# Optimization experiments

Measured on AMD Instinct MI355X. Metric: run time of the kernel, lower is better.

The kernel has to match this reference:

```python
import jax, jax.numpy as jnp
import numpy as np

B, S, D, H = 1, 2048, 1024, 16
HD = D // H
S_SLOPE = 10.0      # soft_thres_layer s
C_MASK = -10000.0   # soft_thres_layer c == masked_bias
ALPHA = 0.0         # config.threshold
W_STD = 0.02        # GPT2 init std for weights


def setup_inputs() -> dict:
    key = jax.random.key(0)
    k1, k2, k3 = jax.random.split(key, 3)
    return {
        "hidden_states": jax.random.normal(k1, (B, S, D), dtype=jnp.float32),
        "c_attn_w": jax.random.normal(k2, (D, 3 * D), dtype=jnp.float32) * W_STD,
        "c_attn_b": jnp.zeros((3 * D,), dtype=jnp.float32),
        "c_proj_w": jax.random.normal(k3, (D, D), dtype=jnp.float32) * W_STD,
        "c_proj_b": jnp.zeros((D,), dtype=jnp.float32),
    }


def reference(hidden_states, c_attn_w, c_attn_b, c_proj_w, c_proj_b):
    # Conv1D: x @ w + b (GPT2 convention: weight is [in, out])
    qkv = hidden_states @ c_attn_w + c_attn_b            # [B,S,3D]
    q, k, v = jnp.split(qkv, 3, axis=-1)

    def split_heads(x):
        return x.reshape(B, S, H, HD).transpose(0, 2, 1, 3)  # [B,H,S,hd]

    q, k, v = split_heads(q), split_heads(k), split_heads(v)

    # prun path: NO 1/sqrt(d) scaling (skipped when self.prun is True)
    w = jnp.einsum("bhqd,bhkd->bhqk", q, k)              # [B,H,S,S]

    causal = jnp.tril(jnp.ones((S, S), dtype=bool))[None, None]
    w = jnp.where(causal, w, C_MASK)

    # soft-threshold pruning: smoothly pushes scores below alpha toward c=-10000
    w = C_MASK + (w - C_MASK) * jax.nn.sigmoid(S_SLOPE * (w - ALPHA))

    a = jax.nn.softmax(w, axis=-1)                        # attn_dropout = identity (eval)
    out = jnp.einsum("bhqk,bhkd->bhqd", a, v)             # [B,H,S,hd]
    out = out.transpose(0, 2, 1, 3).reshape(B, S, D)      # merge heads
    return out @ c_proj_w + c_proj_b                      # resid_dropout = identity
```

## Files before the change

### kernel.cpp

```cpp
#include <hip/hip_runtime.h>


#define S_LEN 2048
#define DM    1024
#define NH    16
#define HD    64
#define SLOPE 10.0f
#define CMASK -10000.0f
#define SP    2080

typedef short s16x4 __attribute__((ext_vector_type(4)));
typedef short s16x8 __attribute__((ext_vector_type(8)));
typedef float f32x4 __attribute__((ext_vector_type(4)));

#define MFMA16(a,b,c) __builtin_amdgcn_mfma_f32_16x16x32_bf16(a,b,c,0,0,0)
#define GLDS16(g,l) __builtin_amdgcn_global_load_lds( \
    (const __attribute__((address_space(1))) void*)(g), \
    (__attribute__((address_space(3))) void*)(l), 16, 0, 0)

__device__ __forceinline__ short f2bf(float f){
    unsigned u = __float_as_uint(f);
    u += 0x7fffu + ((u >> 16) & 1u);
    return (short)(u >> 16);
}
__device__ __forceinline__ float bf2f(short x){
    return __uint_as_float(((unsigned)(unsigned short)x) << 16);
}
struct bfpair { short hi, lo; };
__device__ __forceinline__ bfpair split_bf(float x){
    bfpair r; r.hi = f2bf(x);
    r.lo = f2bf(x - bf2f(r.hi));
    return r;
}

template<int ROWS, int THREADS>
__device__ __forceinline__ void stage_tile(const short* gbase, int rstride,
                                           short* lds, int tid){
#pragma unroll
    for (int it = 0; it < ROWS*8/THREADS; ++it){
        int s = it*THREADS + tid;
        int row = s >> 3, grp = s & 7;
        const short* src = gbase + (size_t)row*rstride + ((grp ^ (row & 7)) << 3);
        GLDS16(src, lds + (size_t)s*8);
    }
}
__device__ __forceinline__ s16x8 frag(const short* lds, int row, int kg){
    return *(const s16x8*)&lds[row*64 + ((kg ^ (row & 7)) << 3)];
}

__global__ __launch_bounds__(256)
void gemm_qkv(const short* __restrict__ Ahg, const short* __restrict__ Alg,
              const short* __restrict__ Bhg, const short* __restrict__ Blg,
              const float* __restrict__ bias,
              short* __restrict__ QHh, short* __restrict__ QHl,
              short* __restrict__ KH,  short* __restrict__ Vb)
{
    __shared__ __align__(16) short Ah_s[128*64];
    __shared__ __align__(16) short Bh_s[128*64];
    __shared__ __align__(16) short Al_s[128*64];
    __shared__ __align__(16) short Bl_s[128*64];

    const int tid = threadIdx.x, lane = tid & 63, wid = tid >> 6;
    const int lr = lane & 15, lg = lane >> 4;
    const int brow = blockIdx.y*128, bcol = blockIdx.x*128;
    const int sec = bcol >> 10;
    const int wm = (wid >> 1)*64, wn = (wid & 1)*64;

    f32x4 acc[4][4];
#pragma unroll
    for (int m = 0; m < 4; ++m)
#pragma unroll
        for (int n = 0; n < 4; ++n) acc[m][n] = (f32x4){0.f,0.f,0.f,0.f};

    for (int k0 = 0; k0 < DM; k0 += 64){
        stage_tile<128,256>(Ahg + (size_t)brow*DM + k0, DM, Ah_s, tid);
        stage_tile<128,256>(Bhg + (size_t)bcol*DM + k0, DM, Bh_s, tid);
        if (sec == 0){
            stage_tile<128,256>(Alg + (size_t)brow*DM + k0, DM, Al_s, tid);
            stage_tile<128,256>(Blg + (size_t)bcol*DM + k0, DM, Bl_s, tid);
        }
        __syncthreads();
#pragma unroll
        for (int kc = 0; kc < 2; ++kc){
            s16x8 ah[4], al[4], bh[4], bl[4];
#pragma unroll
            for (int m = 0; m < 4; ++m)
                ah[m] = frag(Ah_s, wm + m*16 + lr, kc*4 + lg);
#pragma unroll
            for (int n = 0; n < 4; ++n)
                bh[n] = frag(Bh_s, wn + n*16 + lr, kc*4 + lg);
            if (sec == 0){
#pragma unroll
                for (int m = 0; m < 4; ++m)
                    al[m] = frag(Al_s, wm + m*16 + lr, kc*4 + lg);
#pragma unroll
                for (int n = 0; n < 4; ++n)
                    bl[n] = frag(Bl_s, wn + n*16 + lr, kc*4 + lg);
            }
#pragma unroll
            for (int m = 0; m < 4; ++m)
#pragma unroll
                for (int n = 0; n < 4; ++n){
                    acc[m][n] = MFMA16(ah[m], bh[n], acc[m][n]);
                    if (sec == 0){
                        acc[m][n] = MFMA16(ah[m], bl[n], acc[m][n]);
                        acc[m][n] = MFMA16(al[m], bh[n], acc[m][n]);
                    }
                }
        }
        __syncthreads();
    }

#pragma unroll
    for (int m = 0; m < 4; ++m)
#pragma unroll
        for (int n = 0; n < 4; ++n){
            int row  = brow + wm + m*16 + lg*4;
            int gcol = bcol + wn + n*16 + lr;
            float bv = bias[gcol];
            int h0 = (gcol & 1023) >> 6, d = gcol & 63;
#pragma unroll
            for (int v = 0; v < 4; ++v){
                float val = acc[m][n][v] + bv;
                if (sec == 0){
                    bfpair p = split_bf(val);
                    size_t o = ((size_t)h0*S_LEN + row + v)*HD + d;
                    QHh[o] = p.hi; QHl[o] = p.lo;
                } else if (sec == 1){
                    KH[((size_t)h0*S_LEN + row + v)*HD + d] = f2bf(val);
                } else {
                    Vb[(size_t)(row + v)*DM + (gcol & 1023)] = f2bf(val);
                }
            }
        }
}

__global__ __launch_bounds__(256)
void gemm_proj(const short* __restrict__ Ahg, const short* __restrict__ Bhg,
               const float* __restrict__ bias, float* __restrict__ C)
{
    __shared__ __align__(16) short Ah_s[128*64];
    __shared__ __align__(16) short Bh_s[128*64];

    const int tid = threadIdx.x, lane = tid & 63, wid = tid >> 6;
    const int lr = lane & 15, lg = lane >> 4;
    const int brow = blockIdx.y*128, bcol = blockIdx.x*128;
    const int wm = (wid >> 1)*64, wn = (wid & 1)*64;

    f32x4 acc[4][4];
#pragma unroll
    for (int m = 0; m < 4; ++m)
#pragma unroll
        for (int n = 0; n < 4; ++n) acc[m][n] = (f32x4){0.f,0.f,0.f,0.f};

    for (int k0 = 0; k0 < DM; k0 += 64){
        stage_tile<128,256>(Ahg + (size_t)brow*DM + k0, DM, Ah_s, tid);
        stage_tile<128,256>(Bhg + (size_t)bcol*DM + k0, DM, Bh_s, tid);
        __syncthreads();
#pragma unroll
        for (int kc = 0; kc < 2; ++kc){
            s16x8 ah[4], bh[4];
#pragma unroll
            for (int m = 0; m < 4; ++m)
                ah[m] = frag(Ah_s, wm + m*16 + lr, kc*4 + lg);
#pragma unroll
            for (int n = 0; n < 4; ++n)
                bh[n] = frag(Bh_s, wn + n*16 + lr, kc*4 + lg);
#pragma unroll
            for (int m = 0; m < 4; ++m)
#pragma unroll
                for (int n = 0; n < 4; ++n)
                    acc[m][n] = MFMA16(ah[m], bh[n], acc[m][n]);
        }
        __syncthreads();
    }

#pragma unroll
    for (int m = 0; m < 4; ++m)
#pragma unroll
        for (int n = 0; n < 4; ++n){
            int row  = brow + wm + m*16 + lg*4;
            int gcol = bcol + wn + n*16 + lr;
            float bv = bias[gcol];
#pragma unroll
            for (int v = 0; v < 4; ++v)
                C[(size_t)(row + v)*DM + gcol] = acc[m][n][v] + bv;
        }
}

__global__ __launch_bounds__(256)
void split_f32(const float* __restrict__ x, short* __restrict__ h,
               short* __restrict__ l, int n4)
{
    int i = blockIdx.x*256 + threadIdx.x;
    if (i >= n4) return;
    float4 v = *(const float4*)&x[(size_t)i*4];
    bfpair a = split_bf(v.x), b = split_bf(v.y), c = split_bf(v.z), d = split_bf(v.w);
    s16x4 hv, lv;
    hv.x = a.hi; hv.y = b.hi; hv.z = c.hi; hv.w = d.hi;
    lv.x = a.lo; lv.y = b.lo; lv.z = c.lo; lv.w = d.lo;
    *(s16x4*)&h[(size_t)i*4] = hv;
    *(s16x4*)&l[(size_t)i*4] = lv;
}

template<bool SPL>
__global__ __launch_bounds__(256)
void wtrans(const float* __restrict__ W, int N, short* __restrict__ Th,
            short* __restrict__ Tl)
{
    __shared__ float t[64][65];
    const int tid = threadIdx.x;
    const int tn = blockIdx.x*64, tk = blockIdx.y*64;
#pragma unroll
    for (int it = 0; it < 4; ++it){
        int idx = tid + it*256;
        int r = idx >> 4, c4 = (idx & 15)*4;
        float4 v = *(const float4*)&W[(size_t)(tk + r)*N + tn + c4];
        t[r][c4] = v.x; t[r][c4+1] = v.y; t[r][c4+2] = v.z; t[r][c4+3] = v.w;
    }
    __syncthreads();
#pragma unroll
    for (int it = 0; it < 4; ++it){
        int idx = tid + it*256;
        int n = idx >> 4, c4 = (idx & 15)*4;
        s16x4 hv, lv;
#pragma unroll
        for (int j = 0; j < 4; ++j){
            bfpair p = split_bf(t[c4+j][n]);
            hv[j] = p.hi; lv[j] = p.lo;
        }
        *(s16x4*)&Th[(size_t)(tn + n)*DM + tk + c4] = hv;
        if (SPL && tn < DM)
            *(s16x4*)&Tl[(size_t)(tn + n)*DM + tk + c4] = lv;
    }
}

__global__ __launch_bounds__(256)
void vtrans(const short* __restrict__ Vb, short* __restrict__ Vt)
{
    __shared__ short t[64][66];
    const int tid = threadIdx.x;
    const int td = blockIdx.x*64, ts = blockIdx.y*64;
#pragma unroll
    for (int it = 0; it < 4; ++it){
        int idx = tid + it*256;
        int r = idx >> 4, c4 = (idx & 15)*4;
        s16x4 v = *(const s16x4*)&Vb[(size_t)(ts + r)*DM + td + c4];
        t[r][c4] = v.x; t[r][c4+1] = v.y; t[r][c4+2] = v.z; t[r][c4+3] = v.w;
    }
    __syncthreads();
#pragma unroll
    for (int it = 0; it < 4; ++it){
        int idx = tid + it*256;
        int n = idx >> 4, c4 = (idx & 15)*4;
        s16x4 o;
#pragma unroll
        for (int j = 0; j < 4; ++j) o[j] = t[c4+j][n];
        *(s16x4*)&Vt[(size_t)(td + n)*SP + ts + c4] = o;
    }
}

__global__ __launch_bounds__(64)
void sv_partial(const short* __restrict__ Vb, float* __restrict__ PB)
{
    int b = blockIdx.x, h = blockIdx.y, d = threadIdx.x;
    float s = 0.f;
#pragma unroll 8
    for (int k = 0; k < 64; ++k)
        s += bf2f(Vb[(size_t)(b*64 + k)*DM + h*HD + d]);
    PB[((size_t)h*32 + b)*64 + d] = s;
}
__global__ __launch_bounds__(64)
void sv_suffix(const float* __restrict__ PB, float* __restrict__ SSV)
{
    int h = blockIdx.x, d = threadIdx.x;
    float s = 0.f;
    SSV[((size_t)h*33 + 32)*64 + d] = 0.f;
    for (int b = 31; b >= 0; --b){
        s += PB[((size_t)h*32 + b)*64 + d];
        SSV[((size_t)h*33 + b)*64 + d] = s;
    }
}

__global__ __launch_bounds__(64)
void attn_chunk(const short* __restrict__ QHh, const short* __restrict__ QHl,
                const short* __restrict__ KH, const short* __restrict__ Vt,
                short* __restrict__ acc0, short* __restrict__ acc1,
                short* __restrict__ acc2, float* __restrict__ ML)
{
    __shared__ __align__(16) short Ps[16*72];

    const int j = blockIdx.x;
    const int h = (j & 7) + 8*((j >> 3) & 1);
    const int t = j >> 4;
    const int g = (t < 32) ? 0 : (t < 96) ? 1 : (t < 192) ? 2 : 3;
    const int u = t - 16*g*(g+1);
    const int qd = u / (g+1);
    const int qt = 32*g + qd;
    const int chunk = u - qd*(g+1);
    const int diag = qt >> 2;
    const int kv0 = chunk*8;
    const int kv1 = min(kv0 + 8, diag + 1);

    const int lane = threadIdx.x, lr = lane & 15, lg = lane >> 4;
    const int qrow = qt*16 + lg*4;

    const short* qbh = QHh + ((size_t)h*S_LEN + qt*16)*HD;
    const short* qbl = QHl + ((size_t)h*S_LEN + qt*16)*HD;
    s16x8 aqh[2], aql[2];
#pragma unroll
    for (int kc = 0; kc < 2; ++kc){
        aqh[kc] = *(const s16x8*)&qbh[lr*HD + kc*32 + lg*8];
        aql[kc] = *(const s16x8*)&qbl[lr*HD + kc*32 + lg*8];
    }

    float m_run[4], l_run[4];
    f32x4 acc_o[4];
#pragma unroll
    for (int v = 0; v < 4; ++v){ m_run[v] = -1e30f; l_run[v] = 0.f; }
#pragma unroll
    for (int n = 0; n < 4; ++n) acc_o[n] = (f32x4){0.f,0.f,0.f,0.f};

    const short* kb0 = KH + (size_t)h*S_LEN*HD;
    const short* vb0 = Vt + (size_t)(h*HD)*SP;

    for (int kvb = kv0; kvb < kv1; ++kvb){
        const short* kb = kb0 + (size_t)(kvb*64)*HD;
        s16x8 bk[2][4];
#pragma unroll
        for (int kc = 0; kc < 2; ++kc)
#pragma unroll
            for (int n = 0; n < 4; ++n)
                bk[kc][n] = *(const s16x8*)&kb[(n*16 + lr)*HD + kc*32 + lg*8];

        f32x4 sc[4];
#pragma unroll
        for (int n = 0; n < 4; ++n) sc[n] = (f32x4){0.f,0.f,0.f,0.f};
#pragma unroll
        for (int kc = 0; kc < 2; ++kc)
#pragma unroll
            for (int n = 0; n < 4; ++n){
                sc[n] = MFMA16(aqh[kc], bk[kc][n], sc[n]);
                sc[n] = MFMA16(aql[kc], bk[kc][n], sc[n]);
            }

        const short* vb = vb0 + kvb*64;
        s16x8 bv0[4], bv1[4];
#pragma unroll
        for (int n = 0; n < 4; ++n){
            bv0[n] = *(const s16x8*)&vb[(size_t)(16*n + lr)*SP + lg*8];
            bv1[n] = *(const s16x8*)&vb[(size_t)(16*n + lr)*SP + 32 + lg*8];
        }

        float p[4][4], tmax[4];
#pragma unroll
        for (int v = 0; v < 4; ++v) tmax[v] = -1e30f;
        if (kvb == diag){
#pragma unroll
            for (int n = 0; n < 4; ++n){
                int key = kvb*64 + n*16 + lr;
#pragma unroll
                for (int v = 0; v < 4; ++v){
                    float w;
                    if (key > qrow + v) w = CMASK;
                    else {
                        float sv = sc[n][v];
                        float sig = 1.f / (1.f + __expf(-SLOPE*sv));
                        w = CMASK + (sv - CMASK)*sig;
                    }
                    p[n][v] = w;
                    tmax[v] = fmaxf(tmax[v], w);
                }
            }
        } else {
#pragma unroll
            for (int n = 0; n < 4; ++n)
#pragma unroll
                for (int v = 0; v < 4; ++v){
                    float sv = sc[n][v];
                    float sig = 1.f / (1.f + __expf(-SLOPE*sv));
                    float w = CMASK + (sv - CMASK)*sig;
                    p[n][v] = w;
                    tmax[v] = fmaxf(tmax[v], w);
                }
        }
#pragma unroll
        for (int v = 0; v < 4; ++v)
#pragma unroll
            for (int msk = 1; msk < 16; msk <<= 1)
                tmax[v] = fmaxf(tmax[v], __shfl_xor(tmax[v], msk, 64));

        float scale[4], rsum[4];
#pragma unroll
        for (int v = 0; v < 4; ++v){
            float mn = fmaxf(m_run[v], tmax[v]);
            scale[v] = __expf(m_run[v] - mn);
            m_run[v] = mn;
            rsum[v] = 0.f;
        }
#pragma unroll
        for (int n = 0; n < 4; ++n)
#pragma unroll
            for (int v = 0; v < 4; ++v){
                float e = __expf(p[n][v] - m_run[v]);
                p[n][v] = e;
                rsum[v] += e;
            }
#pragma unroll
        for (int v = 0; v < 4; ++v){
#pragma unroll
            for (int msk = 1; msk < 16; msk <<= 1)
                rsum[v] += __shfl_xor(rsum[v], msk, 64);
            l_run[v] = l_run[v]*scale[v] + rsum[v];
        }
#pragma unroll
        for (int n = 0; n < 4; ++n)
#pragma unroll
            for (int v = 0; v < 4; ++v) acc_o[n][v] *= scale[v];

#pragma unroll
        for (int n = 0; n < 4; ++n)
#pragma unroll
            for (int v = 0; v < 4; ++v)
                Ps[(lg*4 + v)*72 + 16*n + lr] = f2bf(p[n][v]);
        asm volatile("s_waitcnt lgkmcnt(0)" ::: "memory");

        s16x8 pa0 = *(const s16x8*)&Ps[lr*72 + lg*8];
        s16x8 pa1 = *(const s16x8*)&Ps[lr*72 + 32 + lg*8];
#pragma unroll
        for (int n = 0; n < 4; ++n){
            acc_o[n] = MFMA16(pa0, bv0[n], acc_o[n]);
            acc_o[n] = MFMA16(pa1, bv1[n], acc_o[n]);
        }
    }

    short* ab = (j < 2048) ? acc0 + (size_t)j*1024
              : (j < 3072) ? acc1 + (size_t)(j-2048)*1024
                           : acc2 + (size_t)(j-3072)*1024;
#pragma unroll
    for (int n = 0; n < 4; ++n)
#pragma unroll
        for (int v = 0; v < 4; ++v)
            ab[(lg*4 + v)*64 + 16*n + lr] = f2bf(acc_o[n][v]);
    if (lr == 0){
#pragma unroll
        for (int v = 0; v < 4; ++v){
            ML[((size_t)j*16 + lg*4 + v)*2 + 0] = m_run[v];
            ML[((size_t)j*16 + lg*4 + v)*2 + 1] = l_run[v];
        }
    }
}

__global__ __launch_bounds__(64)
void attn_merge(const short* __restrict__ acc0, const short* __restrict__ acc1,
                const short* __restrict__ acc2, const float* __restrict__ ML,
                const float* __restrict__ SSV, short* __restrict__ O)
{
    const int b = blockIdx.x;
    const int h = b & 15, qt = b >> 4;
    const int d = threadIdx.x;
    const int g = qt >> 5, C = g + 1;
    const int tbase = (g + 1)*(qt - 16*g);
    const int diag = qt >> 2;
    const float F = (float)(S_LEN - 64*(diag + 1));
    const float svd = SSV[((size_t)h*33 + (diag + 1))*64 + d];

    for (int r = 0; r < 16; ++r){
        float M = -1e30f;
        for (int c = 0; c < C; ++c){
            int job = (tbase + c)*16 + h;
            M = fmaxf(M, ML[((size_t)job*16 + r)*2]);
        }
        float num = 0.f, den = 0.f;
        for (int c = 0; c < C; ++c){
            int job = (tbase + c)*16 + h;
            float m = ML[((size_t)job*16 + r)*2];
            float l = ML[((size_t)job*16 + r)*2 + 1];
            const short* ab = (job < 2048) ? acc0 + (size_t)job*1024
                            : (job < 3072) ? acc1 + (size_t)(job-2048)*1024
                                           : acc2 + (size_t)(job-3072)*1024;
            float e = __expf(m - M);
            num += e * bf2f(ab[r*64 + d]);
            den += e * l;
        }
        float et = __expf(CMASK - M);
        num += et * svd;
        den += et * F;
        O[(size_t)(qt*16 + r)*DM + h*64 + d] = f2bf(num/den);
    }
}

extern "C" void kernel_launch(void* const* d_in, const int* in_sizes, int n_in,
                              void* d_out, int out_size, void* d_ws, size_t ws_size,
                              hipStream_t stream)
{
    (void)in_sizes; (void)n_in; (void)out_size; (void)ws_size;
    const float* hs   = (const float*)d_in[0];
    const float* wqkv = (const float*)d_in[1];
    const float* bqkv = (const float*)d_in[2];
    const float* wprj = (const float*)d_in[3];
    const float* bprj = (const float*)d_in[4];

    char* p = (char*)d_ws;
    short* Ahg  = (short*)(p + (0ull  << 20));
    short* Alg  = (short*)(p + (4ull  << 20));
    short* WqTh = (short*)(p + (8ull  << 20));
    short* WqTl = (short*)(p + (14ull << 20));
    short* QHh  = (short*)(p + (16ull << 20));
    short* QHl  = (short*)(p + (20ull << 20));
    short* KH   = (short*)(p + (24ull << 20));
    short* Vbg  = (short*)(p + (28ull << 20));
    short* VT   = (short*)(p + (32ull << 20));
    float* PB   = (float*)(p + (38ull << 20));
    float* SSV  = (float*)(p + (38ull << 20) + (256ull << 10));
    float* ML   = (float*)(p + (39ull << 20));
    short* O    = Ahg;
    short* WpT  = WqTh;

    split_f32<<<S_LEN*DM/4/256, 256, 0, stream>>>(hs, Ahg, Alg, S_LEN*DM/4);
    wtrans<true><<<dim3(3*DM/64, DM/64), 256, 0, stream>>>(wqkv, 3*DM, WqTh, WqTl);

    gemm_qkv<<<dim3(24, 16), 256, 0, stream>>>(
        Ahg, Alg, WqTh, WqTl, bqkv, QHh, QHl, KH, Vbg);

    wtrans<false><<<dim3(DM/64, DM/64), 256, 0, stream>>>(wprj, DM, WpT, nullptr);
    vtrans<<<dim3(DM/64, S_LEN/64), 256, 0, stream>>>(Vbg, VT);
    sv_partial<<<dim3(32, NH), 64, 0, stream>>>(Vbg, PB);
    sv_suffix<<<NH, 64, 0, stream>>>(PB, SSV);

    attn_chunk<<<5120, 64, 0, stream>>>(QHh, QHl, KH, VT, Alg, WqTl, Vbg, ML);
    attn_merge<<<2048, 64, 0, stream>>>(Alg, WqTl, Vbg, ML, SSV, O);

    gemm_proj<<<dim3(8, 16), 256, 0, stream>>>(O, WpT, bprj, (float*)d_out);
}
```

Measured before the change: 182.1 us.

## Share staged K/V tiles in LDS across four waves per 64-row query block

Attention is restructured from single-wave blocks over 16 query rows into 256-thread blocks covering 64 query rows. Each K/V tile is staged once into shared memory and reused by all four waves, replacing per-wave global loads. The chunk schedule, partial-output layout and merge kernel are remapped to the coarser 64-row tiles. The cost is two barriers per KV step and fewer, larger blocks, which means coarser load balance across the causal triangle.

```diff
diff --git a/kernel.cpp b/kernel.cpp
--- a/kernel.cpp
+++ b/kernel.cpp
@@ -282,31 +282,33 @@
     }
 }
 
-__global__ __launch_bounds__(64)
-void attn_chunk(const short* __restrict__ QHh, const short* __restrict__ QHl,
-                const short* __restrict__ KH, const short* __restrict__ Vt,
-                short* __restrict__ acc0, short* __restrict__ acc1,
-                short* __restrict__ acc2, float* __restrict__ ML)
-{
-    __shared__ __align__(16) short Ps[16*72];
+__global__ __launch_bounds__(256)
+void attn_fwd(const short* __restrict__ QHh, const short* __restrict__ QHl,
+              const short* __restrict__ KH, const short* __restrict__ Vt,
+              short* __restrict__ acc0, short* __restrict__ acc1,
+              short* __restrict__ acc2, float* __restrict__ ML)
+{
+    __shared__ __align__(16) short kh_s[64*64];
+    __shared__ __align__(16) short vt_s[64*64];
+    __shared__ __align__(16) short Ps[4][16*72];
 
     const int j = blockIdx.x;
     const int h = (j & 7) + 8*((j >> 3) & 1);
     const int t = j >> 4;
-    const int g = (t < 32) ? 0 : (t < 96) ? 1 : (t < 192) ? 2 : 3;
-    const int u = t - 16*g*(g+1);
-    const int qd = u / (g+1);
-    const int qt = 32*g + qd;
-    const int chunk = u - qd*(g+1);
-    const int diag = qt >> 2;
-    const int kv0 = chunk*8;
-    const int kv1 = min(kv0 + 8, diag + 1);
-
-    const int lane = threadIdx.x, lr = lane & 15, lg = lane >> 4;
-    const int qrow = qt*16 + lg*4;
-
-    const short* qbh = QHh + ((size_t)h*S_LEN + qt*16)*HD;
-    const short* qbl = QHl + ((size_t)h*S_LEN + qt*16)*HD;
+    int qst, c;
+    if (t < 8)      { qst = t; c = 0; }
+    else if (t < 24){ int u = t - 8;  qst = 8  + (u >> 1); c = u & 1; }
+    else if (t < 48){ int u = t - 24; qst = 16 + u/3;      c = u - (u/3)*3; }
+    else            { int u = t - 48; qst = 24 + (u >> 2); c = u & 3; }
+    const int kv0 = c*8;
+    const int kv1 = min(kv0 + 8, qst + 1);
+
+    const int tid = threadIdx.x, lane = tid & 63, wid = tid >> 6;
+    const int lr = lane & 15, lg = lane >> 4;
+    const int qrow = qst*64 + wid*16 + lg*4;
+
+    const short* qbh = QHh + ((size_t)h*S_LEN + qst*64 + wid*16)*HD;
+    const short* qbl = QHl + ((size_t)h*S_LEN + qst*64 + wid*16)*HD;
     s16x8 aqh[2], aql[2];
 #pragma unroll
     for (int kc = 0; kc < 2; ++kc){
@@ -321,41 +323,28 @@
 #pragma unroll
     for (int n = 0; n < 4; ++n) acc_o[n] = (f32x4){0.f,0.f,0.f,0.f};
 
-    const short* kb0 = KH + (size_t)h*S_LEN*HD;
-    const short* vb0 = Vt + (size_t)(h*HD)*SP;
-
     for (int kvb = kv0; kvb < kv1; ++kvb){
-        const short* kb = kb0 + (size_t)(kvb*64)*HD;
-        s16x8 bk[2][4];
+        __syncthreads();
+        stage_tile<64,256>(KH + ((size_t)h*S_LEN + kvb*64)*HD, HD, kh_s, tid);
+        stage_tile<64,256>(Vt + (size_t)(h*HD)*SP + kvb*64, SP, vt_s, tid);
+        __syncthreads();
+
+        f32x4 sc[4];
+#pragma unroll
+        for (int n = 0; n < 4; ++n) sc[n] = (f32x4){0.f,0.f,0.f,0.f};
 #pragma unroll
         for (int kc = 0; kc < 2; ++kc)
 #pragma unroll
-            for (int n = 0; n < 4; ++n)
-                bk[kc][n] = *(const s16x8*)&kb[(n*16 + lr)*HD + kc*32 + lg*8];
-
-        f32x4 sc[4];
-#pragma unroll
-        for (int n = 0; n < 4; ++n) sc[n] = (f32x4){0.f,0.f,0.f,0.f};
-#pragma unroll
-        for (int kc = 0; kc < 2; ++kc)
-#pragma unroll
             for (int n = 0; n < 4; ++n){
-                sc[n] = MFMA16(aqh[kc], bk[kc][n], sc[n]);
-                sc[n] = MFMA16(aql[kc], bk[kc][n], sc[n]);
+                s16x8 bkh = frag(kh_s, n*16 + lr, kc*4 + lg);
+                sc[n] = MFMA16(aqh[kc], bkh, sc[n]);
+                sc[n] = MFMA16(aql[kc], bkh, sc[n]);
             }
 
-        const short* vb = vb0 + kvb*64;
-        s16x8 bv0[4], bv1[4];
-#pragma unroll
-        for (int n = 0; n < 4; ++n){
-            bv0[n] = *(const s16x8*)&vb[(size_t)(16*n + lr)*SP + lg*8];
-            bv1[n] = *(const s16x8*)&vb[(size_t)(16*n + lr)*SP + 32 + lg*8];
-        }
-
         float p[4][4], tmax[4];
 #pragma unroll
         for (int v = 0; v < 4; ++v) tmax[v] = -1e30f;
-        if (kvb == diag){
+        if (kvb == qst){
 #pragma unroll
             for (int n = 0; n < 4; ++n){
                 int key = kvb*64 + n*16 + lr;
@@ -422,63 +411,68 @@
         for (int n = 0; n < 4; ++n)
 #pragma unroll
             for (int v = 0; v < 4; ++v)
-                Ps[(lg*4 + v)*72 + 16*n + lr] = f2bf(p[n][v]);
+                Ps[wid][(lg*4 + v)*72 + 16*n + lr] = f2bf(p[n][v]);
         asm volatile("s_waitcnt lgkmcnt(0)" ::: "memory");
 
-        s16x8 pa0 = *(const s16x8*)&Ps[lr*72 + lg*8];
-        s16x8 pa1 = *(const s16x8*)&Ps[lr*72 + 32 + lg*8];
+        s16x8 pa0 = *(const s16x8*)&Ps[wid][lr*72 + lg*8];
+        s16x8 pa1 = *(const s16x8*)&Ps[wid][lr*72 + 32 + lg*8];
 #pragma unroll
         for (int n = 0; n < 4; ++n){
-            acc_o[n] = MFMA16(pa0, bv0[n], acc_o[n]);
-            acc_o[n] = MFMA16(pa1, bv1[n], acc_o[n]);
-        }
-    }
-
-    short* ab = (j < 2048) ? acc0 + (size_t)j*1024
-              : (j < 3072) ? acc1 + (size_t)(j-2048)*1024
-                           : acc2 + (size_t)(j-3072)*1024;
+            s16x8 bv0 = frag(vt_s, 16*n + lr, lg);
+            s16x8 bv1 = frag(vt_s, 16*n + lr, 4 + lg);
+            acc_o[n] = MFMA16(pa0, bv0, acc_o[n]);
+            acc_o[n] = MFMA16(pa1, bv1, acc_o[n]);
+        }
+    }
+
+    short* ab = (j < 512) ? acc0 + (size_t)j*4096
+              : (j < 768) ? acc1 + (size_t)(j-512)*4096
+                          : acc2 + (size_t)(j-768)*4096;
 #pragma unroll
     for (int n = 0; n < 4; ++n)
 #pragma unroll
         for (int v = 0; v < 4; ++v)
-            ab[(lg*4 + v)*64 + 16*n + lr] = f2bf(acc_o[n][v]);
+            ab[(wid*16 + lg*4 + v)*64 + 16*n + lr] = f2bf(acc_o[n][v]);
     if (lr == 0){
 #pragma unroll
         for (int v = 0; v < 4; ++v){
-            ML[((size_t)j*16 + lg*4 + v)*2 + 0] = m_run[v];
-            ML[((size_t)j*16 + lg*4 + v)*2 + 1] = l_run[v];
-        }
-    }
-}
-
-__global__ __launch_bounds__(64)
+            ML[((size_t)j*64 + wid*16 + lg*4 + v)*2 + 0] = m_run[v];
+            ML[((size_t)j*64 + wid*16 + lg*4 + v)*2 + 1] = l_run[v];
+        }
+    }
+}
+
+__global__ __launch_bounds__(256)
 void attn_merge(const short* __restrict__ acc0, const short* __restrict__ acc1,
                 const short* __restrict__ acc2, const float* __restrict__ ML,
                 const float* __restrict__ SSV, short* __restrict__ O)
 {
     const int b = blockIdx.x;
-    const int h = b & 15, qt = b >> 4;
-    const int d = threadIdx.x;
-    const int g = qt >> 5, C = g + 1;
-    const int tbase = (g + 1)*(qt - 16*g);
-    const int diag = qt >> 2;
-    const float F = (float)(S_LEN - 64*(diag + 1));
-    const float svd = SSV[((size_t)h*33 + (diag + 1))*64 + d];
-
-    for (int r = 0; r < 16; ++r){
+    const int h = b & 15, qst = b >> 4;
+    const int d = threadIdx.x & 63, rg = threadIdx.x >> 6;
+    const int C = (qst + 8) >> 3;
+    const int tbase = (qst < 8)  ? qst
+                    : (qst < 16) ? 8  + 2*(qst - 8)
+                    : (qst < 24) ? 24 + 3*(qst - 16)
+                                 : 48 + 4*(qst - 24);
+    const float F = (float)(S_LEN - 64*(qst + 1));
+    const float svd = SSV[((size_t)h*33 + (qst + 1))*64 + d];
+
+    for (int i = 0; i < 16; ++i){
+        int r = rg + 4*i;
         float M = -1e30f;
         for (int c = 0; c < C; ++c){
             int job = (tbase + c)*16 + h;
-            M = fmaxf(M, ML[((size_t)job*16 + r)*2]);
+            M = fmaxf(M, ML[((size_t)job*64 + r)*2]);
         }
         float num = 0.f, den = 0.f;
         for (int c = 0; c < C; ++c){
             int job = (tbase + c)*16 + h;
-            float m = ML[((size_t)job*16 + r)*2];
-            float l = ML[((size_t)job*16 + r)*2 + 1];
-            const short* ab = (job < 2048) ? acc0 + (size_t)job*1024
-                            : (job < 3072) ? acc1 + (size_t)(job-2048)*1024
-                                           : acc2 + (size_t)(job-3072)*1024;
+            float m = ML[((size_t)job*64 + r)*2];
+            float l = ML[((size_t)job*64 + r)*2 + 1];
+            const short* ab = (job < 512) ? acc0 + (size_t)job*4096
+                            : (job < 768) ? acc1 + (size_t)(job-512)*4096
+                                          : acc2 + (size_t)(job-768)*4096;
             float e = __expf(m - M);
             num += e * bf2f(ab[r*64 + d]);
             den += e * l;
@@ -486,7 +480,7 @@
         float et = __expf(CMASK - M);
         num += et * svd;
         den += et * F;
-        O[(size_t)(qt*16 + r)*DM + h*64 + d] = f2bf(num/den);
+        O[(size_t)(qst*64 + r)*DM + h*64 + d] = f2bf(num/den);
     }
 }
 
@@ -528,8 +522,8 @@
     sv_partial<<<dim3(32, NH), 64, 0, stream>>>(Vbg, PB);
     sv_suffix<<<NH, 64, 0, stream>>>(PB, SSV);
 
-    attn_chunk<<<5120, 64, 0, stream>>>(QHh, QHl, KH, VT, Alg, WqTl, Vbg, ML);
-    attn_merge<<<2048, 64, 0, stream>>>(Alg, WqTl, Vbg, ML, SSV, O);
+    attn_fwd<<<1280, 256, 0, stream>>>(QHh, QHl, KH, VT, Alg, WqTl, Vbg, ML);
+    attn_merge<<<512, 256, 0, stream>>>(Alg, WqTl, Vbg, ML, SSV, O);
 
     gemm_proj<<<dim3(8, 16), 256, 0, stream>>>(O, WpT, bprj, (float*)d_out);
 }
```

Measured after the change: 181.6 us. Within noise of the previous version (-0.2%).
